# Kernel tuning notes

Hardware: AMD Instinct MI355X
Metric: run time of the kernel (lower is better)

The kernel has to match this reference:

```python
import jax, jax.numpy as jnp
import numpy as np

EMB, HID, OUT = 512, 512, 512

def setup_inputs() -> dict:
    key = jax.random.key(0)
    ks = jax.random.split(key, 7)
    s = 1.0 / np.sqrt(EMB + HID)
    so = 1.0 / np.sqrt(2 * HID)
    return {
        "input_seq": jax.random.normal(ks[0], (32, 512, EMB), dtype=jnp.float32),
        "W_f": jax.random.uniform(ks[1], (EMB + HID, HID), jnp.float32, -s, s),
        "b_f": jax.random.uniform(ks[2], (HID,), jnp.float32, -s, s),
        "W_b": jax.random.uniform(ks[3], (EMB + HID, HID), jnp.float32, -s, s),
        "b_b": jax.random.uniform(ks[4], (HID,), jnp.float32, -s, s),
        "W_o": jax.random.uniform(ks[5], (2 * HID, OUT), jnp.float32, -so, so),
        "b_o": jax.random.uniform(ks[6], (OUT,), jnp.float32, -so, so),
    }

def _rnn_scan(xs, W, b, h0, reverse):
    # split W into input and hidden parts to avoid per-step concat
    Wx, Wh = W[:EMB], W[EMB:]
    def step(h, x_t):
        h_new = jnp.tanh(x_t @ Wx + h @ Wh + b)
        return h_new, h_new
    _, hs = jax.lax.scan(step, h0, xs, reverse=reverse)  # hs: [S, B, H]
    return hs

def reference(input_seq, W_f, b_f, W_b, b_b, W_o, b_o):
    B = input_seq.shape[0]
    xs = jnp.swapaxes(input_seq, 0, 1)  # [S, B, E]
    h0 = jnp.zeros((B, HID), input_seq.dtype)
    hs_f = _rnn_scan(xs, W_f, b_f, h0, reverse=False)   # [S, B, H]
    hs_b = _rnn_scan(xs, W_b, b_b, h0, reverse=True)    # [S, B, H], already time-aligned
    bi = jnp.concatenate([hs_f, hs_b], axis=-1)          # [S, B, 2H]
    out = bi @ W_o + b_o                                 # [S, B, O]
    return jnp.swapaxes(out, 0, 1)                       # [B, S, O]
```

## Files before the change

kernel.cpp:

```cpp
#include <hip/hip_runtime.h>
#include <hip/hip_fp16.h>
#include <stdint.h>

#define SEQ 512
#define HIDN 512

typedef _Float16 h2_t __attribute__((ext_vector_type(2)));
typedef _Float16 h8_t __attribute__((ext_vector_type(8)));
typedef float f4_t __attribute__((ext_vector_type(4)));

__device__ __forceinline__ float fdot2f(uint32_t a, uint32_t b, float c) {
#if __has_builtin(__builtin_amdgcn_fdot2)
  return __builtin_amdgcn_fdot2(__builtin_bit_cast(h2_t, a),
                                __builtin_bit_cast(h2_t, b), c, false);
#else
  h2_t ah = __builtin_bit_cast(h2_t, a);
  h2_t bh = __builtin_bit_cast(h2_t, b);
  return c + (float)ah.x * (float)bh.x + (float)ah.y * (float)bh.y;
#endif
}

__global__ void k_cvt(const float4* __restrict__ src, __half2* __restrict__ dst, int n4) {
  int i = blockIdx.x * blockDim.x + threadIdx.x;
  if (i < n4) {
    float4 v = src[i];
    dst[2 * i]     = __floats2half2_rn(v.x, v.y);
    dst[2 * i + 1] = __floats2half2_rn(v.z, v.w);
  }
}

__global__ void k_transpose_cvt(const float* __restrict__ src, __half* __restrict__ dst,
                                int R, int C) {
  __shared__ float tile[32][33];
  int tx = threadIdx.x, ty = threadIdx.y;
  int c0 = blockIdx.x * 32, r0 = blockIdx.y * 32;
#pragma unroll
  for (int i = 0; i < 4; ++i)
    tile[ty + i * 8][tx] = src[(size_t)(r0 + ty + i * 8) * C + c0 + tx];
  __syncthreads();
#pragma unroll
  for (int i = 0; i < 4; ++i)
    dst[(size_t)(c0 + ty + i * 8) * R + r0 + tx] = __float2half(tile[tx][ty + i * 8]);
}

__global__ __launch_bounds__(256, 2) void k_gemm(
    const __half* __restrict__ A, const __half* __restrict__ Bt,
    const float* __restrict__ bias, float* __restrict__ C,
    int M, int N, int K) {
  __shared__ __align__(16) __half As[128 * 32];
  __shared__ __align__(16) __half Bs[128 * 32];
  const int tid = threadIdx.x;
  const int m0 = blockIdx.x * 128;
  const int n0 = blockIdx.y * 128;
  const int w = tid >> 6;
  const int lane = tid & 63;
  const int wm = (w >> 1) * 64;
  const int wn = (w & 1) * 64;
  const int fr = lane & 15;
  const int q = lane >> 4;
  const int lr = tid >> 2;
  const int lc = tid & 3;
  f4_t acc[4][4];
#pragma unroll
  for (int i = 0; i < 4; ++i)
#pragma unroll
    for (int jj = 0; jj < 4; ++jj) acc[i][jj] = (f4_t)(0.f);

  for (int kk = 0; kk < K; kk += 32) {
    *(uint4*)&As[lr * 32 + lc * 8]        = *(const uint4*)&A[(size_t)(m0 + lr) * K + kk + lc * 8];
    *(uint4*)&As[(64 + lr) * 32 + lc * 8] = *(const uint4*)&A[(size_t)(m0 + 64 + lr) * K + kk + lc * 8];
    *(uint4*)&Bs[lr * 32 + lc * 8]        = *(const uint4*)&Bt[(size_t)(n0 + lr) * K + kk + lc * 8];
    *(uint4*)&Bs[(64 + lr) * 32 + lc * 8] = *(const uint4*)&Bt[(size_t)(n0 + 64 + lr) * K + kk + lc * 8];
    __syncthreads();
    h8_t af[4], bf[4];
#pragma unroll
    for (int i = 0; i < 4; ++i) {
      af[i] = *(const h8_t*)&As[(wm + i * 16 + fr) * 32 + q * 8];
      bf[i] = *(const h8_t*)&Bs[(wn + i * 16 + fr) * 32 + q * 8];
    }
#pragma unroll
    for (int i = 0; i < 4; ++i)
#pragma unroll
      for (int jj = 0; jj < 4; ++jj)
        acc[i][jj] = __builtin_amdgcn_mfma_f32_16x16x32_f16(af[i], bf[jj], acc[i][jj], 0, 0, 0);
    __syncthreads();
  }
#pragma unroll
  for (int i = 0; i < 4; ++i) {
    const int row0 = m0 + wm + i * 16 + q * 4;
#pragma unroll
    for (int jj = 0; jj < 4; ++jj) {
      const int col = n0 + wn + jj * 16 + fr;
      const float bv = bias[col];
#pragma unroll
      for (int r = 0; r < 4; ++r)
        C[(size_t)(row0 + r) * N + col] = acc[i][jj][r] + bv;
    }
  }
}

__global__ __launch_bounds__(1024) void k_rnn(
    const __half* __restrict__ WhT_f, const __half* __restrict__ WhT_b,
    const float* __restrict__ A_f, const float* __restrict__ A_b,
    __half* __restrict__ bi) {
  __shared__ __align__(16) uint4 ldsw4[9 * 1024];
  __shared__ __align__(16) __half hbuf[2][HIDN];
  __shared__ float psum[2][HIDN];
  const int t = threadIdx.x;
  const int j = t & 511;
  const int half = t >> 9;
  const int d = blockIdx.x & 1;
  const int b = blockIdx.x >> 1;
  const __half* WhT = d ? WhT_b : WhT_f;
  const float* A = (d ? A_b : A_f) + (size_t)b * SEQ * HIDN;
  __half* birow = bi + (size_t)b * SEQ * 1024 + d * HIDN + j;

  const uint4* wrow4 = (const uint4*)(WhT + (size_t)j * HIDN);
  uint4 wv[23];
#pragma unroll
  for (int i = 0; i < 23; ++i) wv[i] = wrow4[half * 32 + i];
#pragma unroll
  for (int p = 0; p < 9; ++p) ldsw4[p * 1024 + t] = wrow4[half * 32 + 23 + p];
  if (half == 0) hbuf[0][j] = __float2half(0.f);
  __syncthreads();

  const int tstep = d ? -1 : 1;
  int tt = d ? (SEQ - 1) : 0;
  float a_next = A[(size_t)tt * HIDN + j];
  int cur = 0;
  for (int s = 0; s < SEQ; ++s) {
    float a_cur = a_next;
    int tn = tt + tstep;
    tn = tn < 0 ? 0 : (tn > SEQ - 1 ? SEQ - 1 : tn);
    a_next = A[(size_t)tn * HIDN + j];
    const uint4* hp = (const uint4*)hbuf[cur] + half * 32;
    float acc0 = 0.f, acc1 = 0.f, acc2 = 0.f, acc3 = 0.f;
#pragma unroll
    for (int i = 0; i < 23; ++i) {
      uint4 hv = hp[i];
      acc0 = fdot2f(hv.x, wv[i].x, acc0);
      acc1 = fdot2f(hv.y, wv[i].y, acc1);
      acc2 = fdot2f(hv.z, wv[i].z, acc2);
      acc3 = fdot2f(hv.w, wv[i].w, acc3);
    }
#pragma unroll
    for (int p = 0; p < 9; ++p) {
      uint4 hv = hp[23 + p];
      uint4 lw = ldsw4[p * 1024 + t];
      acc0 = fdot2f(hv.x, lw.x, acc0);
      acc1 = fdot2f(hv.y, lw.y, acc1);
      acc2 = fdot2f(hv.z, lw.z, acc2);
      acc3 = fdot2f(hv.w, lw.w, acc3);
    }
    psum[half][j] = (acc0 + acc1) + (acc2 + acc3);
    __syncthreads();
    float p = psum[0][j] + psum[1][j] + a_cur;
    float ap = fabsf(p);
    float e = __expf(2.f * ap);
    float th = 1.f - 2.f * __builtin_amdgcn_rcpf(e + 1.f);
    float h = copysignf(th, p);
    __half hh = __float2half(h);
    hbuf[cur ^ 1][j] = hh;
    if (half == 0) birow[(size_t)tt * 1024] = hh;
    cur ^= 1;
    tt += tstep;
    __syncthreads();
  }
}

extern "C" void kernel_launch(void* const* d_in, const int* in_sizes, int n_in,
                              void* d_out, int out_size, void* d_ws, size_t ws_size,
                              hipStream_t stream) {
  const float* input_seq = (const float*)d_in[0];
  const float* W_f = (const float*)d_in[1];
  const float* b_f = (const float*)d_in[2];
  const float* W_b = (const float*)d_in[3];
  const float* b_b = (const float*)d_in[4];
  const float* W_o = (const float*)d_in[5];
  const float* b_o = (const float*)d_in[6];
  float* out = (float*)d_out;

  char* ws = (char*)d_ws;
  __half* Xh    = (__half*)(ws);
  float*  A_f   = (float*)(ws + 16777216);
  float*  A_b   = (float*)(ws + 50331648);
  __half* bi    = (__half*)(ws + 83886080);
  __half* WxT_f = (__half*)(ws + 117440512);
  __half* WxT_b = (__half*)(ws + 117964800);
  __half* WhT_f = (__half*)(ws + 118489088);
  __half* WhT_b = (__half*)(ws + 119013376);
  __half* WoT   = (__half*)(ws + 119537664);

  k_cvt<<<8192, 256, 0, stream>>>((const float4*)input_seq, (__half2*)Xh, 2097152);
  dim3 tb(32, 8);
  k_transpose_cvt<<<dim3(16, 16), tb, 0, stream>>>(W_f,          WxT_f, 512, 512);
  k_transpose_cvt<<<dim3(16, 16), tb, 0, stream>>>(W_f + 262144, WhT_f, 512, 512);
  k_transpose_cvt<<<dim3(16, 16), tb, 0, stream>>>(W_b,          WxT_b, 512, 512);
  k_transpose_cvt<<<dim3(16, 16), tb, 0, stream>>>(W_b + 262144, WhT_b, 512, 512);
  k_transpose_cvt<<<dim3(16, 32), tb, 0, stream>>>(W_o,          WoT, 1024, 512);

  k_gemm<<<dim3(128, 4), 256, 0, stream>>>(Xh, WxT_f, b_f, A_f, 16384, 512, 512);
  k_gemm<<<dim3(128, 4), 256, 0, stream>>>(Xh, WxT_b, b_b, A_b, 16384, 512, 512);

  k_rnn<<<64, 1024, 0, stream>>>(WhT_f, WhT_b, A_f, A_b, bi);

  k_gemm<<<dim3(128, 4), 256, 0, stream>>>(bi, WoT, b_o, out, 16384, 512, 1024);
}
```

Measured before the change: 997.1 us.

## Restructure RNN kernel to 512 threads with register weights plus streamed global remainder

The recurrent kernel moves from 1024 threads, each handling half a dot product with a psum reduction through shared memory and an extra barrier, to 512 threads that each compute a full hidden unit. 40 of the 64 weight chunks stay in registers, and the remaining 24 are streamed from global memory (L2) every step with software-pipelined loads behind sched_barriers. A new prep kernel packs the Wh matrices into this interleaved layout. This drops one barrier and the partial-sum exchange per step, but adds global-memory weight traffic on every timestep and doubles serial dot-product work per thread.

```diff
diff --git a/kernel.cpp b/kernel.cpp
--- a/kernel.cpp
+++ b/kernel.cpp
@@ -41,6 +41,25 @@
 #pragma unroll
   for (int i = 0; i < 4; ++i)
     dst[(size_t)(c0 + ty + i * 8) * R + r0 + tx] = __float2half(tile[tx][ty + i * 8]);
+}
+
+__global__ void k_wprep(const float* __restrict__ W, uint4* __restrict__ dst) {
+  int idx = blockIdx.x * 256 + threadIdx.x;
+  int i = idx >> 9;
+  int j = idx & 511;
+  const float* src = W + (size_t)(512 + i * 8) * 512 + j;
+  uint32_t u0 = __builtin_bit_cast(uint32_t, __floats2half2_rn(src[0],        src[512]));
+  uint32_t u1 = __builtin_bit_cast(uint32_t, __floats2half2_rn(src[1024],     src[1536]));
+  uint32_t u2 = __builtin_bit_cast(uint32_t, __floats2half2_rn(src[2048],     src[2560]));
+  uint32_t u3 = __builtin_bit_cast(uint32_t, __floats2half2_rn(src[3072],     src[3584]));
+  uint4 v; v.x = u0; v.y = u1; v.z = u2; v.w = u3;
+  if (i < 40) {
+    dst[i * 512 + j] = v;
+  } else {
+    int ii = i - 40;
+    int g = ii >> 2, c = ii & 3;
+    dst[40 * 512 + ((size_t)(g * 512 + j) * 4 + c)] = v;
+  }
 }
 
 __global__ __launch_bounds__(256, 2) void k_gemm(
@@ -99,72 +118,99 @@
   }
 }
 
-__global__ __launch_bounds__(1024) void k_rnn(
-    const __half* __restrict__ WhT_f, const __half* __restrict__ WhT_b,
+#define LOADG(SX, G) do {                                          \
+    SX[0] = Wstr[((size_t)((G) * 512 + j)) * 4 + 0];               \
+    SX[1] = Wstr[((size_t)((G) * 512 + j)) * 4 + 1];               \
+    SX[2] = Wstr[((size_t)((G) * 512 + j)) * 4 + 2];               \
+    SX[3] = Wstr[((size_t)((G) * 512 + j)) * 4 + 3];               \
+  } while (0)
+
+#define CONS(SX, CB) do {                                          \
+    uint4 hv;                                                      \
+    hv = hp[(CB) + 0];                                             \
+    c0 = fdot2f(hv.x, SX[0].x, c0); c1 = fdot2f(hv.y, SX[0].y, c1);\
+    c2 = fdot2f(hv.z, SX[0].z, c2); c3 = fdot2f(hv.w, SX[0].w, c3);\
+    hv = hp[(CB) + 1];                                             \
+    c0 = fdot2f(hv.x, SX[1].x, c0); c1 = fdot2f(hv.y, SX[1].y, c1);\
+    c2 = fdot2f(hv.z, SX[1].z, c2); c3 = fdot2f(hv.w, SX[1].w, c3);\
+    hv = hp[(CB) + 2];                                             \
+    c0 = fdot2f(hv.x, SX[2].x, c0); c1 = fdot2f(hv.y, SX[2].y, c1);\
+    c2 = fdot2f(hv.z, SX[2].z, c2); c3 = fdot2f(hv.w, SX[2].w, c3);\
+    hv = hp[(CB) + 3];                                             \
+    c0 = fdot2f(hv.x, SX[3].x, c0); c1 = fdot2f(hv.y, SX[3].y, c1);\
+    c2 = fdot2f(hv.z, SX[3].z, c2); c3 = fdot2f(hv.w, SX[3].w, c3);\
+  } while (0)
+
+__global__ __launch_bounds__(512, 1) void k_rnn(
+    const uint4* __restrict__ Wp_f, const uint4* __restrict__ Wp_b,
     const float* __restrict__ A_f, const float* __restrict__ A_b,
     __half* __restrict__ bi) {
-  __shared__ __align__(16) uint4 ldsw4[9 * 1024];
   __shared__ __align__(16) __half hbuf[2][HIDN];
-  __shared__ float psum[2][HIDN];
-  const int t = threadIdx.x;
-  const int j = t & 511;
-  const int half = t >> 9;
+  const int j = threadIdx.x;
   const int d = blockIdx.x & 1;
   const int b = blockIdx.x >> 1;
-  const __half* WhT = d ? WhT_b : WhT_f;
+  const uint4* Wp = d ? Wp_b : Wp_f;
   const float* A = (d ? A_b : A_f) + (size_t)b * SEQ * HIDN;
-  __half* birow = bi + (size_t)b * SEQ * 1024 + d * HIDN + j;
-
-  const uint4* wrow4 = (const uint4*)(WhT + (size_t)j * HIDN);
-  uint4 wv[23];
-#pragma unroll
-  for (int i = 0; i < 23; ++i) wv[i] = wrow4[half * 32 + i];
-#pragma unroll
-  for (int p = 0; p < 9; ++p) ldsw4[p * 1024 + t] = wrow4[half * 32 + 23 + p];
-  if (half == 0) hbuf[0][j] = __float2half(0.f);
+  __half* bip = bi + (size_t)b * SEQ * 1024 + d * HIDN + j;
+  const uint4* Wres = Wp;
+  const uint4* Wstr = Wp + 40 * 512;
+
+  uint4 wv[40];
+#pragma unroll
+  for (int i = 0; i < 40; ++i) wv[i] = Wres[i * 512 + j];
+
+  hbuf[0][j] = __float2half(0.f);
   __syncthreads();
 
   const int tstep = d ? -1 : 1;
   int tt = d ? (SEQ - 1) : 0;
   float a_next = A[(size_t)tt * HIDN + j];
   int cur = 0;
+#pragma unroll 1
   for (int s = 0; s < SEQ; ++s) {
     float a_cur = a_next;
     int tn = tt + tstep;
     tn = tn < 0 ? 0 : (tn > SEQ - 1 ? SEQ - 1 : tn);
     a_next = A[(size_t)tn * HIDN + j];
-    const uint4* hp = (const uint4*)hbuf[cur] + half * 32;
-    float acc0 = 0.f, acc1 = 0.f, acc2 = 0.f, acc3 = 0.f;
-#pragma unroll
-    for (int i = 0; i < 23; ++i) {
+    const uint4* hp = (const uint4*)hbuf[cur];
+
+    uint4 s0[4], s1[4], s2[4], s3[4], s4[4], s5[4];
+    LOADG(s0, 0);
+    LOADG(s1, 1);
+    __builtin_amdgcn_sched_barrier(0);
+
+    float c0 = 0.f, c1 = 0.f, c2 = 0.f, c3 = 0.f;
+#pragma unroll
+    for (int i = 0; i < 40; ++i) {
       uint4 hv = hp[i];
-      acc0 = fdot2f(hv.x, wv[i].x, acc0);
-      acc1 = fdot2f(hv.y, wv[i].y, acc1);
-      acc2 = fdot2f(hv.z, wv[i].z, acc2);
-      acc3 = fdot2f(hv.w, wv[i].w, acc3);
+      c0 = fdot2f(hv.x, wv[i].x, c0);
+      c1 = fdot2f(hv.y, wv[i].y, c1);
+      c2 = fdot2f(hv.z, wv[i].z, c2);
+      c3 = fdot2f(hv.w, wv[i].w, c3);
     }
-#pragma unroll
-    for (int p = 0; p < 9; ++p) {
-      uint4 hv = hp[23 + p];
-      uint4 lw = ldsw4[p * 1024 + t];
-      acc0 = fdot2f(hv.x, lw.x, acc0);
-      acc1 = fdot2f(hv.y, lw.y, acc1);
-      acc2 = fdot2f(hv.z, lw.z, acc2);
-      acc3 = fdot2f(hv.w, lw.w, acc3);
-    }
-    psum[half][j] = (acc0 + acc1) + (acc2 + acc3);
-    __syncthreads();
-    float p = psum[0][j] + psum[1][j] + a_cur;
+    __builtin_amdgcn_sched_barrier(0);
+    CONS(s0, 40); LOADG(s2, 2);
+    __builtin_amdgcn_sched_barrier(0);
+    CONS(s1, 44); LOADG(s3, 3);
+    __builtin_amdgcn_sched_barrier(0);
+    CONS(s2, 48); LOADG(s4, 4);
+    __builtin_amdgcn_sched_barrier(0);
+    CONS(s3, 52); LOADG(s5, 5);
+    __builtin_amdgcn_sched_barrier(0);
+    CONS(s4, 56);
+    CONS(s5, 60);
+
+    float p = (c0 + c1) + (c2 + c3) + a_cur;
     float ap = fabsf(p);
     float e = __expf(2.f * ap);
     float th = 1.f - 2.f * __builtin_amdgcn_rcpf(e + 1.f);
     float h = copysignf(th, p);
     __half hh = __float2half(h);
     hbuf[cur ^ 1][j] = hh;
-    if (half == 0) birow[(size_t)tt * 1024] = hh;
+    bip[(size_t)tt * 1024] = hh;
+    __syncthreads();
     cur ^= 1;
     tt += tstep;
-    __syncthreads();
   }
 }
 
@@ -187,22 +233,22 @@
   __half* bi    = (__half*)(ws + 83886080);
   __half* WxT_f = (__half*)(ws + 117440512);
   __half* WxT_b = (__half*)(ws + 117964800);
-  __half* WhT_f = (__half*)(ws + 118489088);
-  __half* WhT_b = (__half*)(ws + 119013376);
+  uint4*  Wp_f  = (uint4*)(ws + 118489088);
+  uint4*  Wp_b  = (uint4*)(ws + 119013376);
   __half* WoT   = (__half*)(ws + 119537664);
 
   k_cvt<<<8192, 256, 0, stream>>>((const float4*)input_seq, (__half2*)Xh, 2097152);
   dim3 tb(32, 8);
-  k_transpose_cvt<<<dim3(16, 16), tb, 0, stream>>>(W_f,          WxT_f, 512, 512);
-  k_transpose_cvt<<<dim3(16, 16), tb, 0, stream>>>(W_f + 262144, WhT_f, 512, 512);
-  k_transpose_cvt<<<dim3(16, 16), tb, 0, stream>>>(W_b,          WxT_b, 512, 512);
-  k_transpose_cvt<<<dim3(16, 16), tb, 0, stream>>>(W_b + 262144, WhT_b, 512, 512);
-  k_transpose_cvt<<<dim3(16, 32), tb, 0, stream>>>(W_o,          WoT, 1024, 512);
+  k_transpose_cvt<<<dim3(16, 16), tb, 0, stream>>>(W_f, WxT_f, 512, 512);
+  k_transpose_cvt<<<dim3(16, 16), tb, 0, stream>>>(W_b, WxT_b, 512, 512);
+  k_transpose_cvt<<<dim3(16, 32), tb, 0, stream>>>(W_o, WoT, 1024, 512);
+  k_wprep<<<128, 256, 0, stream>>>(W_f, Wp_f);
+  k_wprep<<<128, 256, 0, stream>>>(W_b, Wp_b);
 
   k_gemm<<<dim3(128, 4), 256, 0, stream>>>(Xh, WxT_f, b_f, A_f, 16384, 512, 512);
   k_gemm<<<dim3(128, 4), 256, 0, stream>>>(Xh, WxT_b, b_b, A_b, 16384, 512, 512);
 
-  k_rnn<<<64, 1024, 0, stream>>>(WhT_f, WhT_b, A_f, A_b, bi);
+  k_rnn<<<64, 512, 0, stream>>>(Wp_f, Wp_b, A_f, A_b, bi);
 
   k_gemm<<<dim3(128, 4), 256, 0, stream>>>(bi, WoT, b_o, out, 16384, 512, 1024);
 }
```

Measured after the change: 1.693 ms. +69.8%, slower.
